# Optimization experiments

Measured on AMD Instinct MI355X. Metric: run time of the kernel, lower is better.

Reference implementation:

```python
import jax, jax.numpy as jnp
import numpy as np

N = 100000      # nodes
E = 1600000     # directed edges (avg degree 16)
D_IN, D_H, D_OUT = 128, 128, 1


def gcn_conv(x, src, dst, W, b, n):
    """PyG GCNConv: out = D^{-1/2} (A+I) D^{-1/2} X W + b.
    src/dst already include self-loops. deg counted on dst (in-degree)."""
    h = x @ W                                            # [n, d_out]
    deg = jax.ops.segment_sum(jnp.ones(src.shape[0], h.dtype), dst, num_segments=n)
    dinv = jax.lax.rsqrt(jnp.maximum(deg, 1.0))          # deg >= 1 (self loops)
    norm = dinv[src] * dinv[dst]                         # [e]
    msg = h[src] * norm[:, None]                         # gather + scale, [e, d_out]
    out = jax.ops.segment_sum(msg, dst, num_segments=n)  # scatter-add, [n, d_out]
    return out + b


def setup_inputs() -> dict:
    key = jax.random.key(0)
    ks = jax.random.split(key, 8)
    x = jax.random.normal(ks[0], (N, D_IN), dtype=jnp.float32)
    edge_index = jax.random.randint(ks[1], (2, E), 0, N, dtype=jnp.int64)

    def glorot(k, fan_in, fan_out):
        s = jnp.sqrt(6.0 / (fan_in + fan_out)).astype(jnp.float32)
        return jax.random.uniform(k, (fan_in, fan_out), jnp.float32, -s, s)

    W0 = glorot(ks[2], D_IN, D_H)
    b0 = jnp.zeros((D_H,), jnp.float32)
    W1 = glorot(ks[3], D_H, D_H)
    b1 = jnp.zeros((D_H,), jnp.float32)
    W2 = glorot(ks[4], D_H, D_OUT)
    b2 = jnp.zeros((D_OUT,), jnp.float32)
    return {"x": x, "edge_index": edge_index,
            "W0": W0, "b0": b0, "W1": W1, "b1": b1, "W2": W2, "b2": b2}


def reference(x, edge_index, W0, b0, W1, b1, W2, b2):
    n = x.shape[0]
    loops = jnp.arange(n, dtype=edge_index.dtype)
    src = jnp.concatenate([edge_index[0], loops])
    dst = jnp.concatenate([edge_index[1], loops])
    # dropout is identity in eval mode
    h = jax.nn.relu(gcn_conv(x, src, dst, W0, b0, n))
    h = jax.nn.relu(gcn_conv(h, src, dst, W1, b1, n))
    out = gcn_conv(h, src, dst, W2, b2, n)
    return jax.nn.sigmoid(out)
```

## Files before the change

kernel.cpp:

```cpp
#include <hip/hip_runtime.h>
#include <cstddef>

#define D 128
#define BW_LOG 9
#define BW 512
#define CHUNK 8192
#define CAP 16384
#define GP 136
typedef unsigned int uint;
typedef unsigned short ushort;
typedef unsigned char uchar;

typedef __attribute__((ext_vector_type(8))) short bf16x8;
typedef __attribute__((ext_vector_type(4))) float f32x4;

static __device__ __forceinline__ uint bf16r(float x) {
  uint u = __float_as_uint(x);
  return (u + 0x7fffu + ((u >> 16) & 1u)) >> 16;
}
static __device__ __forceinline__ uint pack2(float a, float b) {
  return bf16r(a) | (bf16r(b) << 16);
}
static __device__ __forceinline__ void acc_u8x8(const uint2 v, float rs, float* a) {
  a[0] = fmaf((float)(v.x & 0xffu), rs, a[0]);
  a[1] = fmaf((float)((v.x >> 8) & 0xffu), rs, a[1]);
  a[2] = fmaf((float)((v.x >> 16) & 0xffu), rs, a[2]);
  a[3] = fmaf((float)(v.x >> 24), rs, a[3]);
  a[4] = fmaf((float)(v.y & 0xffu), rs, a[4]);
  a[5] = fmaf((float)((v.y >> 8) & 0xffu), rs, a[5]);
  a[6] = fmaf((float)((v.y >> 16) & 0xffu), rs, a[6]);
  a[7] = fmaf((float)(v.y >> 24), rs, a[7]);
}

__global__ void k_wsplit(const float* __restrict__ W0, const float* __restrict__ W1,
                         const float* __restrict__ b0, const float* __restrict__ b1,
                         const float* __restrict__ W2, ushort* __restrict__ out,
                         float* __restrict__ bp, int* __restrict__ bmeta) {
  int idx = blockIdx.x * 256 + threadIdx.x;
  if (idx < 1024) bmeta[idx] = 0;
  if (idx < 128) {
    int p = (idx & 15) * 8 + (idx >> 4);
    bp[p] = b0[idx];
    bp[128 + p] = b1[idx];
    bp[256 + p] = W2[idx];
  }
  if (idx >= 32768) return;
  int lay = idx >> 14;
  int rem = idx & 16383;
  int col = rem >> 7, k = rem & 127;
  const float* W = lay ? W1 : W0;
  float w = W[k * D + col];
  uint hb = bf16r(w);
  float hf = __uint_as_float(hb << 16);
  int ks = lay ? ((k & 15) * 8 + (k >> 4)) : k;
  out[lay * 32768 + col * 128 + ks] = (ushort)hb;
  out[lay * 32768 + 16384 + col * 128 + ks] = (ushort)bf16r(w - hf);
}

__global__ __launch_bounds__(512)
void k_bscatter(const int* __restrict__ ei, int* __restrict__ cursor,
                int* __restrict__ pk, int e, int nb) {
  __shared__ int h[256], lbase[256], gpos[256], lcur[256], s2[256];
  __shared__ int staged[CHUNK];
  __shared__ uchar sbid[CHUNK];
  int t = threadIdx.x;
  if (t < 256) h[t] = 0;
  __syncthreads();
  int base = blockIdx.x * CHUNK;
  int m = min(CHUNK, e - base);
  int sv[16], dv[16];
#pragma unroll
  for (int k = 0; k < 16; ++k) {
    int i = t + k * 512;
    sv[k] = 0; dv[k] = 0;
    if (i < m) {
      sv[k] = ei[base + i];
      dv[k] = ei[e + base + i];
      atomicAdd(&h[dv[k] >> BW_LOG], 1);
    }
  }
  __syncthreads();
  if (t < 256) s2[t] = h[t];
  __syncthreads();
  for (int d = 1; d < 256; d <<= 1) {
    int x = 0;
    if (t < 256 && t >= d) x = s2[t - d];
    __syncthreads();
    if (t < 256) s2[t] += x;
    __syncthreads();
  }
  if (t < 256) {
    lbase[t] = s2[t] - h[t];
    lcur[t] = s2[t] - h[t];
    gpos[t] = (t < nb && h[t]) ? atomicAdd(&cursor[t], h[t]) : 0;
  }
  __syncthreads();
#pragma unroll
  for (int k = 0; k < 16; ++k) {
    int i = t + k * 512;
    if (i < m) {
      int b = dv[k] >> BW_LOG;
      int p = atomicAdd(&lcur[b], 1);
      staged[p] = sv[k] | ((dv[k] & (BW - 1)) << 17);
      sbid[p] = (uchar)b;
    }
  }
  __syncthreads();
  for (int i = t; i < m; i += 512) {
    int b = sbid[i];
    int dst = gpos[b] + (i - lbase[b]);
    if (dst < CAP) pk[(size_t)b * CAP + dst] = staged[i];
  }
}

__global__ void k_bscan(const int* __restrict__ cursor, int* __restrict__ bbase,
                        int* __restrict__ off, int nb, int n, int e) {
  __shared__ int s[256];
  int t = threadIdx.x;
  int v = (t < nb) ? cursor[t] : 0;
  s[t] = v;
  __syncthreads();
  for (int d = 1; d < 256; d <<= 1) {
    int x = (t >= d) ? s[t - d] : 0;
    __syncthreads();
    s[t] += x;
    __syncthreads();
  }
  if (t < nb) bbase[t] = s[t] - v;
  if (t == 0) {
    bbase[nb] = e;
    off[n] = e;
  }
}

__global__ __launch_bounds__(1024)
void k_bfinal(const int* __restrict__ bbase, const int* __restrict__ pk,
              int* __restrict__ off, float* __restrict__ dinv,
              int* __restrict__ csr, int n, int nb) {
  __shared__ int sc[BW];
  __shared__ int lcur[BW];
  const int b = blockIdx.x;
  const int t = threadIdx.x;
  const int e0 = bbase[b];
  const int cnt = bbase[b + 1] - e0;
  const int* seg = pk + (size_t)b * CAP;
  const int node0 = b << BW_LOG;
  if (t < BW) { sc[t] = 0; lcur[t] = 0; }
  __syncthreads();
  for (int i = t; i < cnt; i += 1024) atomicAdd(&sc[(seg[i] >> 17) & (BW - 1)], 1);
  __syncthreads();
  int c0 = (t < BW) ? sc[t] : 0;
  for (int d = 1; d < BW; d <<= 1) {
    int v0 = (t < BW && t >= d) ? sc[t - d] : 0;
    __syncthreads();
    if (t < BW) sc[t] += v0;
    __syncthreads();
  }
  if (t < BW) {
    int na = node0 + t;
    if (na < n) {
      off[na] = e0 + sc[t] - c0;
      dinv[na] = rsqrtf((float)c0 + 1.0f);
    }
    sc[t] -= c0;
  }
  __syncthreads();
  for (int i = t; i < cnt; i += 1024) {
    int v = seg[i];
    int dl = (v >> 17) & (BW - 1);
    int p = atomicAdd(&lcur[dl], 1);
    csr[e0 + sc[dl] + p] = v & 0x1FFFF;
  }
}

template <bool BF16A>
__global__ __launch_bounds__(256)
void k_mgemm(const void* __restrict__ Xv, const ushort* __restrict__ Wht,
             const ushort* __restrict__ Wlt, const float* __restrict__ dinv,
             uchar* __restrict__ Aq, float* __restrict__ rs, int n, int nstrips) {
  __shared__ __align__(16) ushort Wh[128 * GP];
  const int tid = threadIdx.x;

  for (int c = tid; c < 2048; c += 256)
    *(uint4*)(&Wh[(c >> 4) * GP + (c & 15) * 8]) = *(const uint4*)(Wht + c * 8);
  __syncthreads();

  const int wv = tid >> 6;
  const int l = tid & 63;
  const int lr = l & 15;
  const int lk = (l >> 4) * 8;

  const char* Xf = (const char*)Xv;
  const char* Xb = (const char*)Xv;

  for (int strip = blockIdx.x * 4 + wv; strip < nstrips; strip += gridDim.x * 4) {
    const int row0 = strip * 16;
    f32x4 acc[8];
#pragma unroll
    for (int t = 0; t < 8; ++t) acc[t] = (f32x4){0.f, 0.f, 0.f, 0.f};

    const int arow = row0 + lr;
    const bool av = (arow < n);

#pragma unroll
    for (int ks = 0; ks < 4; ++ks) {
      const int k0 = ks * 32 + lk;
      bf16x8 ahv;
      if (BF16A) {
        if (av) {
          ahv = *(const bf16x8*)(Xb + ((uint)arow * (D * 2) + (uint)k0 * 2));
        } else {
          union { bf16x8 v; ushort a[8]; } z;
#pragma unroll
          for (int j = 0; j < 8; ++j) z.a[j] = 0;
          ahv = z.v;
        }
      } else {
        union { bf16x8 v; ushort a[8]; } ah;
        if (av) {
          const f32x4* ap = (const f32x4*)(Xf + ((uint)arow * (D * 4) + (uint)k0 * 4));
          f32x4 u0 = __builtin_nontemporal_load(ap);
          f32x4 u1 = __builtin_nontemporal_load(ap + 1);
          ah.a[0] = (ushort)bf16r(u0.x);
          ah.a[1] = (ushort)bf16r(u0.y);
          ah.a[2] = (ushort)bf16r(u0.z);
          ah.a[3] = (ushort)bf16r(u0.w);
          ah.a[4] = (ushort)bf16r(u1.x);
          ah.a[5] = (ushort)bf16r(u1.y);
          ah.a[6] = (ushort)bf16r(u1.z);
          ah.a[7] = (ushort)bf16r(u1.w);
        } else {
#pragma unroll
          for (int j = 0; j < 8; ++j) ah.a[j] = 0;
        }
        ahv = ah.v;
      }
#pragma unroll
      for (int nt = 0; nt < 8; ++nt) {
        bf16x8 bh = *(const bf16x8*)(&Wh[(nt * 16 + lr) * GP + k0]);
        bf16x8 bl = *(const bf16x8*)(Wlt + (size_t)(nt * 16 + lr) * D + k0);
        acc[nt] = __builtin_amdgcn_mfma_f32_16x16x32_bf16(ahv, bh, acc[nt], 0, 0, 0);
        acc[nt] = __builtin_amdgcn_mfma_f32_16x16x32_bf16(ahv, bl, acc[nt], 0, 0, 0);
      }
    }

#pragma unroll
    for (int r = 0; r < 4; ++r) {
      int row = row0 + (l >> 4) * 4 + r;
      float di = (row < n) ? dinv[row] : 0.f;
      float v[8];
      float am = 0.f;
#pragma unroll
      for (int nt = 0; nt < 8; ++nt) {
        v[nt] = acc[nt][r] * di;
        am = fmaxf(am, fabsf(v[nt]));
      }
      am = fmaxf(am, __shfl_xor(am, 1));
      am = fmaxf(am, __shfl_xor(am, 2));
      am = fmaxf(am, __shfl_xor(am, 4));
      am = fmaxf(am, __shfl_xor(am, 8));
      float inv = (am > 0.f) ? 127.f / am : 0.f;
      uint q[8];
#pragma unroll
      for (int nt = 0; nt < 8; ++nt) q[nt] = (uint)(int)rintf(fmaf(v[nt], inv, 128.f));
      uint w0 = q[0] | (q[1] << 8) | (q[2] << 16) | (q[3] << 24);
      uint w1 = q[4] | (q[5] << 8) | (q[6] << 16) | (q[7] << 24);
      if (row < n) {
        *(uint2*)(Aq + ((uint)row * D + (uint)lr * 8)) = make_uint2(w0, w1);
        if (lr == 0) rs[row] = am * (1.f / 127.f);
      }
    }
  }
}

template <bool FUSE_DOT>
__global__ __launch_bounds__(256)
void k_gather(const int* __restrict__ off, const int* __restrict__ csr,
              const float* __restrict__ dinv, const uchar* __restrict__ Aq,
              const float* __restrict__ rsc, ushort* __restrict__ Bb,
              const float* __restrict__ bias, const float* __restrict__ W2,
              float* __restrict__ ss, int n) {
  const int wid = blockIdx.x * 4 + (threadIdx.x >> 6);
  if (wid >= n) return;
  const int lane = threadIdx.x & 63;
  const int q = lane >> 4;
  const int li = lane & 15;
  const int c = li << 3;

  float a[8];
#pragma unroll
  for (int k = 0; k < 8; ++k) a[k] = 0.f;
  float ssc = 0.f;

  if (q == 0) {
    uint2 sv = *(const uint2*)(Aq + (((uint)wid << 7) | (uint)c));
    float rs = rsc[wid];
    acc_u8x8(sv, rs, a);
    ssc += rs;
  }

  const int o0 = off[wid], o1 = off[wid + 1];
  for (int j0 = o0; j0 < o1; j0 += 64) {
    int sj = 0;
    float rsj = 0.f;
    if (j0 + lane < o1) {
      sj = csr[j0 + lane];
      rsj = rsc[sj];
    }
    const int m = min(64, o1 - j0);
    const int nst = (m + 3) >> 2;
#pragma unroll 8
    for (int t = 0; t < nst; ++t) {
      int idx = (t << 2) + q;
      int s = __shfl(sj, idx);
      float rs = __shfl(rsj, idx);
      if (idx < m) {
        uint2 v = *(const uint2*)(Aq + (((uint)s << 7) | (uint)c));
        acc_u8x8(v, rs, a);
        ssc += rs;
      }
    }
  }

#pragma unroll
  for (int k = 0; k < 8; ++k) a[k] = fmaf(-128.f, ssc, a[k]);
#pragma unroll
  for (int k = 0; k < 8; ++k) {
    a[k] += __shfl_xor(a[k], 16);
    a[k] += __shfl_xor(a[k], 32);
  }

  const float di = dinv[wid];
  float4 bb0 = *(const float4*)(bias + c);
  float4 bb1 = *(const float4*)(bias + c + 4);
  float v0 = fmaxf(a[0] * di + bb0.x, 0.f);
  float v1 = fmaxf(a[1] * di + bb0.y, 0.f);
  float v2 = fmaxf(a[2] * di + bb0.z, 0.f);
  float v3 = fmaxf(a[3] * di + bb0.w, 0.f);
  float v4 = fmaxf(a[4] * di + bb1.x, 0.f);
  float v5 = fmaxf(a[5] * di + bb1.y, 0.f);
  float v6 = fmaxf(a[6] * di + bb1.z, 0.f);
  float v7 = fmaxf(a[7] * di + bb1.w, 0.f);

  if (FUSE_DOT) {
    float4 w0 = *(const float4*)(W2 + c);
    float4 w1 = *(const float4*)(W2 + c + 4);
    float p = v0 * w0.x + v1 * w0.y + v2 * w0.z + v3 * w0.w +
              v4 * w1.x + v5 * w1.y + v6 * w1.z + v7 * w1.w;
    p += __shfl_xor(p, 1);
    p += __shfl_xor(p, 2);
    p += __shfl_xor(p, 4);
    p += __shfl_xor(p, 8);
    if (lane == 0) ss[wid] = p * di;
  } else {
    if (lane < 16) {
      uint4 w;
      w.x = pack2(v0, v1);
      w.y = pack2(v2, v3);
      w.z = pack2(v4, v5);
      w.w = pack2(v6, v7);
      *(uint4*)(Bb + ((uint)wid * D + (uint)c)) = w;
    }
  }
}

__global__ void k_gather_scalar(const int* __restrict__ off, const int* __restrict__ csr,
                                const float* __restrict__ dinv, const float* __restrict__ ss,
                                const float* __restrict__ b2, float* __restrict__ out, int n) {
  int i = blockIdx.x * 256 + threadIdx.x;
  if (i >= n) return;
  float acc = ss[i];
  int j = off[i], o1 = off[i + 1];
  float a0 = 0.f, a1 = 0.f, a2 = 0.f, a3 = 0.f;
  for (; j + 4 <= o1; j += 4) {
    int s0 = csr[j], s1 = csr[j + 1], s2 = csr[j + 2], s3 = csr[j + 3];
    a0 += ss[s0];
    a1 += ss[s1];
    a2 += ss[s2];
    a3 += ss[s3];
  }
  for (; j < o1; ++j) a0 += ss[csr[j]];
  acc += (a0 + a1) + (a2 + a3);
  float v = acc * dinv[i] + b2[0];
  out[i] = 1.f / (1.f + expf(-v));
}

extern "C" void kernel_launch(void* const* d_in, const int* in_sizes, int n_in,
                              void* d_out, int out_size, void* d_ws, size_t ws_size,
                              hipStream_t stream) {
  const float* x  = (const float*)d_in[0];
  const int*   ei = (const int*)d_in[1];
  const float* W0 = (const float*)d_in[2];
  const float* b0 = (const float*)d_in[3];
  const float* W1 = (const float*)d_in[4];
  const float* b1 = (const float*)d_in[5];
  const float* W2 = (const float*)d_in[6];
  const float* b2 = (const float*)d_in[7];
  float* out = (float*)d_out;

  const int n = in_sizes[0] / D;
  const int e = in_sizes[1] / 2;
  const int ep = (e + 3) & ~3;
  const int nb = (n + BW - 1) / BW;
  const int nstrips = (n + 15) / 16;
  const size_t np = ((size_t)n + 256) / 256 * 256;

  float* ws = (float*)d_ws;
  int*    off    = (int*)ws;
  float*  dinv   = ws + np;
  float*  ss     = ws + 2 * np;
  int*    bmeta  = (int*)(ws + 3 * np);
  int*    cursor = bmeta;
  int*    bbase  = bmeta + 300;
  ushort* wsp    = (ushort*)(ws + 3 * np + 1024);
  float*  bp     = ws + 3 * np + 1024 + 32768;
  int*    csr    = (int*)(bp + 512);
  int*    pk     = csr + ep;
  uchar*  Aq0    = (uchar*)(pk + (size_t)nb * CAP);
  float*  rs0    = (float*)(Aq0 + (size_t)n * D);
  ushort* Bb     = (ushort*)(rs0 + np);
  uchar*  Aq1    = (uchar*)(Bb + (size_t)n * D);
  float*  rs1    = (float*)(Aq1 + (size_t)n * D);

  const ushort* W0h = wsp;
  const ushort* W0l = wsp + 16384;
  const ushort* W1h = wsp + 32768;
  const ushort* W1l = wsp + 49152;
  const float*  b0p = bp;
  const float*  b1p = bp + 128;
  const float*  W2p = bp + 256;

  const int g256n = (n + 255) / 256;
  const int ggath = (n + 3) / 4;
  const int gchnk = (e + CHUNK - 1) / CHUNK;
  const int ggemm = (nstrips + 3) / 4 < 1024 ? (nstrips + 3) / 4 : 1024;

  k_wsplit<<<128, 256, 0, stream>>>(W0, W1, b0, b1, W2, (ushort*)wsp, bp, bmeta);
  k_bscatter<<<gchnk, 512, 0, stream>>>(ei, cursor, pk, e, nb);
  k_bscan<<<1, 256, 0, stream>>>(cursor, bbase, off, nb, n, e);
  k_bfinal<<<nb, 1024, 0, stream>>>(bbase, pk, off, dinv, csr, n, nb);

  k_mgemm<false><<<ggemm, 256, 0, stream>>>(x, W0h, W0l, dinv, Aq0, rs0, n, nstrips);
  k_gather<false><<<ggath, 256, 0, stream>>>(off, csr, dinv, Aq0, rs0, Bb, b0p, nullptr, nullptr, n);

  k_mgemm<true><<<ggemm, 256, 0, stream>>>(Bb, W1h, W1l, dinv, Aq1, rs1, n, nstrips);
  k_gather<true><<<ggath, 256, 0, stream>>>(off, csr, dinv, Aq1, rs1, nullptr, b1p, W2p, ss, n);

  k_gather_scalar<<<g256n, 256, 0, stream>>>(off, csr, dinv, ss, b2, out, n);
}
```

Measured before the change: 267.3 us.

## Fold bucket scan into bfinal, drop gather bounds check, use plain loads

Removes the single-block k_bscan launch: every k_bfinal block now redoes the 256-entry prefix scan over the bucket cursors in shared memory and derives its own base offset, with block 0 writing off[n]. Separately, the gather inner loop drops its idx<m guard, relying on lanes past the valid range holding index 0 and weight 0 so they add nothing, and its unroll factor goes from 8 to 4. The first GEMM switches its fp32 input reads from nontemporal to ordinary loads. These trade one kernel launch and some branch overhead for redundant scan work per block and a few wasted loads of row 0.

```diff
diff --git a/kernel.cpp b/kernel.cpp
--- a/kernel.cpp
+++ b/kernel.cpp
@@ -113,40 +113,29 @@
   }
 }
 
-__global__ void k_bscan(const int* __restrict__ cursor, int* __restrict__ bbase,
-                        int* __restrict__ off, int nb, int n, int e) {
-  __shared__ int s[256];
-  int t = threadIdx.x;
-  int v = (t < nb) ? cursor[t] : 0;
-  s[t] = v;
-  __syncthreads();
-  for (int d = 1; d < 256; d <<= 1) {
-    int x = (t >= d) ? s[t - d] : 0;
-    __syncthreads();
-    s[t] += x;
-    __syncthreads();
-  }
-  if (t < nb) bbase[t] = s[t] - v;
-  if (t == 0) {
-    bbase[nb] = e;
-    off[n] = e;
-  }
-}
-
 __global__ __launch_bounds__(1024)
-void k_bfinal(const int* __restrict__ bbase, const int* __restrict__ pk,
+void k_bfinal(const int* __restrict__ cursor, const int* __restrict__ pk,
               int* __restrict__ off, float* __restrict__ dinv,
               int* __restrict__ csr, int n, int nb) {
+  __shared__ int cs[256];
   __shared__ int sc[BW];
   __shared__ int lcur[BW];
   const int b = blockIdx.x;
   const int t = threadIdx.x;
-  const int e0 = bbase[b];
-  const int cnt = bbase[b + 1] - e0;
+  if (t < 256) cs[t] = (t < nb) ? cursor[t] : 0;
+  if (t < BW) { sc[t] = 0; lcur[t] = 0; }
+  __syncthreads();
+  for (int d = 1; d < 256; d <<= 1) {
+    int v = (t < 256 && t >= d) ? cs[t - d] : 0;
+    __syncthreads();
+    if (t < 256) cs[t] += v;
+    __syncthreads();
+  }
+  const int cnt = cursor[b];
+  const int e0 = cs[b] - cnt;
+  if (b == 0 && t == 0) off[n] = cs[255];
   const int* seg = pk + (size_t)b * CAP;
   const int node0 = b << BW_LOG;
-  if (t < BW) { sc[t] = 0; lcur[t] = 0; }
-  __syncthreads();
   for (int i = t; i < cnt; i += 1024) atomicAdd(&sc[(seg[i] >> 17) & (BW - 1)], 1);
   __syncthreads();
   int c0 = (t < BW) ? sc[t] : 0;
@@ -219,8 +208,8 @@
         union { bf16x8 v; ushort a[8]; } ah;
         if (av) {
           const f32x4* ap = (const f32x4*)(Xf + ((uint)arow * (D * 4) + (uint)k0 * 4));
-          f32x4 u0 = __builtin_nontemporal_load(ap);
-          f32x4 u1 = __builtin_nontemporal_load(ap + 1);
+          f32x4 u0 = *ap;
+          f32x4 u1 = *(ap + 1);
           ah.a[0] = (ushort)bf16r(u0.x);
           ah.a[1] = (ushort)bf16r(u0.y);
           ah.a[2] = (ushort)bf16r(u0.z);
@@ -309,16 +298,14 @@
     }
     const int m = min(64, o1 - j0);
     const int nst = (m + 3) >> 2;
-#pragma unroll 8
+#pragma unroll 4
     for (int t = 0; t < nst; ++t) {
       int idx = (t << 2) + q;
       int s = __shfl(sj, idx);
       float rs = __shfl(rsj, idx);
-      if (idx < m) {
-        uint2 v = *(const uint2*)(Aq + (((uint)s << 7) | (uint)c));
-        acc_u8x8(v, rs, a);
-        ssc += rs;
-      }
+      uint2 v = *(const uint2*)(Aq + (((uint)s << 7) | (uint)c));
+      acc_u8x8(v, rs, a);
+      ssc += rs;
     }
   }
 
@@ -411,7 +398,6 @@
   float*  ss     = ws + 2 * np;
   int*    bmeta  = (int*)(ws + 3 * np);
   int*    cursor = bmeta;
-  int*    bbase  = bmeta + 300;
   ushort* wsp    = (ushort*)(ws + 3 * np + 1024);
   float*  bp     = ws + 3 * np + 1024 + 32768;
   int*    csr    = (int*)(bp + 512);
@@ -437,8 +423,7 @@
 
   k_wsplit<<<128, 256, 0, stream>>>(W0, W1, b0, b1, W2, (ushort*)wsp, bp, bmeta);
   k_bscatter<<<gchnk, 512, 0, stream>>>(ei, cursor, pk, e, nb);
-  k_bscan<<<1, 256, 0, stream>>>(cursor, bbase, off, nb, n, e);
-  k_bfinal<<<nb, 1024, 0, stream>>>(bbase, pk, off, dinv, csr, n, nb);
+  k_bfinal<<<nb, 1024, 0, stream>>>(cursor, pk, off, dinv, csr, n, nb);
 
   k_mgemm<false><<<ggemm, 256, 0, stream>>>(x, W0h, W0l, dinv, Aq0, rs0, n, nstrips);
   k_gather<false><<<ggath, 256, 0, stream>>>(off, csr, dinv, Aq0, rs0, Bb, b0p, nullptr, nullptr, n);
```

New measurement: 256.6 us. -4.0%, faster.
